# Kernel optimization log

Measured on AMD Instinct MI355X. Metric: run time of the kernel, lower is better.

Reference implementation:

```python
import jax, jax.numpy as jnp
import numpy as np

N, E = 50000, 600000
IN_DIM, HID, OUT = 512, 256, 64
NEG_SLOPE = 0.2  # pyg GATConv default negative_slope


def setup_inputs() -> dict:
    key = jax.random.key(0)
    ks = jax.random.split(key, 6)
    features = jax.random.normal(ks[0], (N, IN_DIM), jnp.float32)
    edge_index = jax.random.randint(ks[1], (2, E), 0, N)
    W1 = jax.random.normal(ks[2], (IN_DIM, HID), jnp.float32) * (1.0 / np.sqrt(IN_DIM))
    W2 = jax.random.normal(ks[3], (HID, OUT), jnp.float32) * (1.0 / np.sqrt(HID))
    att_src = jax.random.normal(ks[4], (HID,), jnp.float32) * 0.1
    att_dst = jax.random.normal(ks[5], (HID,), jnp.float32) * 0.1
    return {"features": features, "W1": W1, "W2": W2,
            "att_src": att_src, "att_dst": att_dst, "edge_index": edge_index}


def _gat_propagate(h_pre, a_src, a_dst, src, dst, n):
    """STAGATE GATConv message passing (heads=1, concat=False, no self loops).

    Per-edge logit = leaky_relu(alpha_src[src] + alpha_dst[dst]),
    softmax over edges sharing the same dst, scatter-add of weighted src feats.
    """
    logits = jax.nn.leaky_relu(a_src[src] + a_dst[dst], NEG_SLOPE)        # [E]
    m = jax.ops.segment_max(logits, dst, num_segments=n)                   # [N]
    ex = jnp.exp(logits - m[dst])                                          # [E]
    denom = jax.ops.segment_sum(ex, dst, num_segments=n)                   # [N]
    w = ex / (denom[dst] + 1e-16)                                          # [E], pyg softmax eps
    return jax.ops.segment_sum(h_pre[src] * w[:, None], dst, num_segments=n)  # [N, C]


def reference(features, W1, W2, att_src, att_dst, edge_index):
    src, dst = edge_index[0], edge_index[1]
    n = features.shape[0]
    # conv1: attention computed and cached (self.attentions)
    hp1 = features @ W1                      # [N, HID]
    a_s = hp1 @ att_src                      # [N] per-node src attention score
    a_d = hp1 @ att_dst                      # [N] per-node dst attention score
    h1 = jax.nn.elu(_gat_propagate(hp1, a_s, a_d, src, dst, n))
    # conv2: attention=False -> plain linear
    h2 = h1 @ W2                             # [N, OUT]
    # conv3: weights = conv2.lin_src.T, tied_attention = conv1.attentions
    hp3 = h2 @ W2.T                          # [N, HID]
    h3 = jax.nn.elu(_gat_propagate(hp3, a_s, a_d, src, dst, n))
    # conv4: weights = conv1.lin_src.T, attention=False
    h4 = h3 @ W1.T                           # [N, IN_DIM]
    return (h2, h4)
```

## Files before the change

### kernel.cpp

```cpp
#include <hip/hip_runtime.h>
#include <hip/hip_bf16.h>
#include <cstdint>
#include <cstddef>

#define IN_DIM 512
#define HID 256
#define OUTD 64
#define NEG_SLOPE 0.2f

typedef __attribute__((ext_vector_type(8))) __bf16 bfrag_t;
typedef __attribute__((ext_vector_type(4))) float facc_t;
typedef __attribute__((ext_vector_type(4))) unsigned int u32x4;

__device__ __forceinline__ float bf2f(unsigned short u) {
  return __uint_as_float(((unsigned int)u) << 16);
}
__device__ __forceinline__ unsigned short f2bf(float f) {
  unsigned int x = __float_as_uint(f);
  x = (x + 0x7FFFu + ((x >> 16) & 1u)) >> 16;
  return (unsigned short)x;
}

#define GLOAD_LDS16(g, l)                                              \
  __builtin_amdgcn_global_load_lds(                                    \
      (const __attribute__((address_space(1))) void*)(g),              \
      (__attribute__((address_space(3))) void*)(l), 16, 0, 0)

template <int BM, int BN>
__global__ __launch_bounds__(256) void gemm_bt(const unsigned short* __restrict__ A,
                                               const unsigned short* __restrict__ B,
                                               void* __restrict__ Craw,
                                               unsigned short* __restrict__ Cb,
                                               int M, int N, int K, int c32) {
  constexpr int FM = BM / 32, FN = BN / 32;
  constexpr int RT = BM + BN;
  __shared__ __align__(16) unsigned short lds[RT * 32];

  const int bm0 = blockIdx.x * BM;
  const int bn0 = blockIdx.y * BN;
  const int tid = threadIdx.x;
  const int lane = tid & 63;
  const int wave = tid >> 6;
  const int wrow = (wave >> 1) * (BM / 2);
  const int wcol = (wave & 1) * (BN / 2);
  const int lr = lane & 15;
  const int quad = lane >> 4;
  const int swz = (quad ^ (lr & 3)) << 3;

  facc_t acc[FM][FN];
#pragma unroll
  for (int i = 0; i < FM; ++i)
#pragma unroll
    for (int j = 0; j < FN; ++j) acc[i][j] = (facc_t){0.f, 0.f, 0.f, 0.f};

  for (int k0 = 0; k0 < K; k0 += 32) {
    __syncthreads();
#pragma unroll
    for (int t = wave; t < RT / 16; t += 4) {
      const int r0 = t * 16;
      const int row = r0 + (lane >> 2);
      const int seg = (lane & 3) ^ (row & 3);
      const unsigned short* g;
      if (r0 < BM) {
        int gm = bm0 + row;
        if (gm >= M) gm = M - 1;
        g = A + (size_t)gm * K + k0 + seg * 8;
      } else {
        g = B + (size_t)(bn0 + row - BM) * K + k0 + seg * 8;
      }
      GLOAD_LDS16(g, lds + t * 512);
    }
    __syncthreads();

    bfrag_t a[FM], b[FN];
#pragma unroll
    for (int i = 0; i < FM; ++i)
      a[i] = *(const bfrag_t*)&lds[(wrow + i * 16 + lr) * 32 + swz];
#pragma unroll
    for (int j = 0; j < FN; ++j)
      b[j] = *(const bfrag_t*)&lds[(BM + wcol + j * 16 + lr) * 32 + swz];
#pragma unroll
    for (int i = 0; i < FM; ++i)
#pragma unroll
      for (int j = 0; j < FN; ++j)
        acc[i][j] = __builtin_amdgcn_mfma_f32_16x16x32_bf16(a[i], b[j], acc[i][j], 0, 0, 0);
  }

#pragma unroll
  for (int i = 0; i < FM; ++i)
#pragma unroll
    for (int r = 0; r < 4; ++r) {
      const int grow = bm0 + wrow + i * 16 + quad * 4 + r;
      if (grow < M) {
#pragma unroll
        for (int j = 0; j < FN; ++j) {
          const int gcol = bn0 + wcol + j * 16 + lr;
          const float v = acc[i][j][r];
          if (c32) ((float*)Craw)[(size_t)grow * N + gcol] = v;
          else ((unsigned short*)Craw)[(size_t)grow * N + gcol] = f2bf(v);
          if (Cb) Cb[(size_t)grow * N + gcol] = f2bf(v);
        }
      }
    }
}

__global__ void cvt_feat(const float* __restrict__ in, unsigned short* __restrict__ out,
                         int n8) {
  const int i = blockIdx.x * 256 + threadIdx.x;
  if (i >= n8) return;
  const float4 f0 = ((const float4*)in)[i * 2];
  const float4 f1 = ((const float4*)in)[i * 2 + 1];
  u32x4 pk;
  pk.x = (unsigned int)f2bf(f0.x) | ((unsigned int)f2bf(f0.y) << 16);
  pk.y = (unsigned int)f2bf(f0.z) | ((unsigned int)f2bf(f0.w) << 16);
  pk.z = (unsigned int)f2bf(f1.x) | ((unsigned int)f2bf(f1.y) << 16);
  pk.w = (unsigned int)f2bf(f1.z) | ((unsigned int)f2bf(f1.w) << 16);
  ((u32x4*)out)[i] = pk;
}

__global__ void cvt_straight(const float* __restrict__ in, unsigned short* __restrict__ out,
                             int nelem) {
  const int i = blockIdx.x * 256 + threadIdx.x;
  if (i < nelem) out[i] = f2bf(in[i]);
}

__global__ void transpose_cvt(const float* __restrict__ in, unsigned short* __restrict__ out,
                              int R, int C) {
  const int idx = blockIdx.x * 256 + threadIdx.x;
  if (idx >= R * C) return;
  const int r = idx / C, c = idx % C;
  out[(size_t)c * R + r] = f2bf(in[idx]);
}

__global__ __launch_bounds__(256) void rowdot(const unsigned short* __restrict__ hp,
                                              const float* __restrict__ att_s,
                                              const float* __restrict__ att_d,
                                              float* __restrict__ as_, float* __restrict__ ad_,
                                              int n) {
  const int node = blockIdx.x * 4 + (threadIdx.x >> 6);
  if (node >= n) return;
  const int lane = threadIdx.x & 63;
  const unsigned short* row = hp + (size_t)node * HID + (lane << 2);
  float s = 0.f, d = 0.f;
#pragma unroll
  for (int j = 0; j < 4; ++j) {
    const float h = bf2f(row[j]);
    s += h * att_s[(lane << 2) + j];
    d += h * att_d[(lane << 2) + j];
  }
  for (int off = 32; off > 0; off >>= 1) {
    s += __shfl_down(s, off);
    d += __shfl_down(d, off);
  }
  if (lane == 0) { as_[node] = s; ad_[node] = d; }
}

__global__ void init_nodes(float* __restrict__ denom, int* __restrict__ deg, int n) {
  const int i = blockIdx.x * 256 + threadIdx.x;
  if (i < n) {
    denom[i] = 0.f;
    deg[i] = 0;
  }
}

__global__ void edge_pass1(const int* __restrict__ src, const int* __restrict__ dst,
                           const float* __restrict__ as_, const float* __restrict__ ad_,
                           float* __restrict__ eexp, float* __restrict__ denom,
                           int* __restrict__ deg, int E, int n) {
  const int e = blockIdx.x * 256 + threadIdx.x;
  if (e >= E) return;
  const int s = src[e], d = dst[e];
  if ((unsigned)s >= (unsigned)n || (unsigned)d >= (unsigned)n) return;
  float l = as_[s] + ad_[d];
  l = l > 0.f ? l : NEG_SLOPE * l;
  const float ex = expf(fminf(l, 60.f));
  eexp[e] = ex;
  atomicAdd(&denom[d], ex);
  atomicAdd(&deg[d], 1);
}

__global__ __launch_bounds__(256) void scan_reduce(const int* __restrict__ deg,
                                                   int* __restrict__ bsum, int n) {
  __shared__ int ws4[4];
  const int tid = threadIdx.x, lane = tid & 63, wid = tid >> 6;
  const int base = blockIdx.x * 2048 + tid * 8;
  int s = 0;
#pragma unroll
  for (int j = 0; j < 8; ++j) {
    const int i = base + j;
    if (i < n) s += deg[i];
  }
  for (int off = 32; off > 0; off >>= 1) s += __shfl_down(s, off);
  if (lane == 0) ws4[wid] = s;
  __syncthreads();
  if (tid == 0) bsum[blockIdx.x] = ws4[0] + ws4[1] + ws4[2] + ws4[3];
}

__global__ __launch_bounds__(256) void scan_final(const int* __restrict__ deg,
                                                  const int* __restrict__ bsum,
                                                  int* __restrict__ row_ptr,
                                                  int* __restrict__ cursor, int n) {
  __shared__ int wsum[4];
  __shared__ int blockoff;
  const int tid = threadIdx.x, lane = tid & 63, wid = tid >> 6;
  if (wid == 0) {
    int v = (lane < blockIdx.x) ? bsum[lane] : 0;
    for (int off = 32; off > 0; off >>= 1) v += __shfl_down(v, off);
    if (lane == 0) blockoff = v;
  }
  const int base = blockIdx.x * 2048 + tid * 8;
  int v[8], s = 0;
#pragma unroll
  for (int j = 0; j < 8; ++j) {
    const int i = base + j;
    v[j] = (i < n) ? deg[i] : 0;
    s += v[j];
  }
  int ws = s;
  for (int off = 1; off < 64; off <<= 1) {
    const int t = __shfl_up(ws, off);
    if (lane >= off) ws += t;
  }
  if (lane == 63) wsum[wid] = ws;
  __syncthreads();
  int woff = 0;
  for (int w_ = 0; w_ < wid; ++w_) woff += wsum[w_];
  int run = blockoff + woff + (ws - s);
#pragma unroll
  for (int j = 0; j < 8; ++j) {
    const int i = base + j;
    if (i < n) {
      cursor[i] = run;
      row_ptr[i + 1] = run + v[j];
    }
    run += v[j];
  }
  if (blockIdx.x == 0 && tid == 0) row_ptr[0] = 0;
}

__global__ void edge_scatter(const int* __restrict__ src, const int* __restrict__ dst,
                             const float* __restrict__ eexp, const float* __restrict__ denom,
                             int* __restrict__ cursor, int* __restrict__ csr_src,
                             float* __restrict__ csr_w, int E, int n) {
  const int e = blockIdx.x * 256 + threadIdx.x;
  if (e >= E) return;
  const int s = src[e], d = dst[e];
  if ((unsigned)s >= (unsigned)n || (unsigned)d >= (unsigned)n) return;
  const float w = eexp[e] / (denom[d] + 1e-16f);
  const int pos = atomicAdd(&cursor[d], 1);
  csr_src[pos] = s;
  csr_w[pos] = w;
}

__global__ __launch_bounds__(256) void gat_prop(const unsigned short* __restrict__ hpre,
                                                const int* __restrict__ row_ptr,
                                                const int* __restrict__ csr_src,
                                                const float* __restrict__ csr_w,
                                                unsigned short* __restrict__ out, int n) {
  const int node = blockIdx.x * 4 + (threadIdx.x >> 6);
  if (node >= n) return;
  const int lane = threadIdx.x & 63;
  const int beg = row_ptr[node], end = row_ptr[node + 1];
  const unsigned short* rowbase = hpre + (size_t)(lane << 2);
  float a0 = 0.f, a1 = 0.f, a2 = 0.f, a3 = 0.f;
  int e = beg;
  for (; e + 4 <= end; e += 4) {
    const int s0 = csr_src[e], s1 = csr_src[e + 1], s2 = csr_src[e + 2], s3 = csr_src[e + 3];
    const float w0 = csr_w[e], w1 = csr_w[e + 1], w2 = csr_w[e + 2], w3 = csr_w[e + 3];
    const uint2 v0 = *(const uint2*)(rowbase + (size_t)s0 * HID);
    const uint2 v1 = *(const uint2*)(rowbase + (size_t)s1 * HID);
    const uint2 v2 = *(const uint2*)(rowbase + (size_t)s2 * HID);
    const uint2 v3 = *(const uint2*)(rowbase + (size_t)s3 * HID);
    a0 += w0 * bf2f((unsigned short)(v0.x & 0xffffu)) + w1 * bf2f((unsigned short)(v1.x & 0xffffu))
        + w2 * bf2f((unsigned short)(v2.x & 0xffffu)) + w3 * bf2f((unsigned short)(v3.x & 0xffffu));
    a1 += w0 * bf2f((unsigned short)(v0.x >> 16)) + w1 * bf2f((unsigned short)(v1.x >> 16))
        + w2 * bf2f((unsigned short)(v2.x >> 16)) + w3 * bf2f((unsigned short)(v3.x >> 16));
    a2 += w0 * bf2f((unsigned short)(v0.y & 0xffffu)) + w1 * bf2f((unsigned short)(v1.y & 0xffffu))
        + w2 * bf2f((unsigned short)(v2.y & 0xffffu)) + w3 * bf2f((unsigned short)(v3.y & 0xffffu));
    a3 += w0 * bf2f((unsigned short)(v0.y >> 16)) + w1 * bf2f((unsigned short)(v1.y >> 16))
        + w2 * bf2f((unsigned short)(v2.y >> 16)) + w3 * bf2f((unsigned short)(v3.y >> 16));
  }
  for (; e < end; ++e) {
    const int s = csr_src[e];
    const float w = csr_w[e];
    const uint2 v = *(const uint2*)(rowbase + (size_t)s * HID);
    a0 += w * bf2f((unsigned short)(v.x & 0xffffu));
    a1 += w * bf2f((unsigned short)(v.x >> 16));
    a2 += w * bf2f((unsigned short)(v.y & 0xffffu));
    a3 += w * bf2f((unsigned short)(v.y >> 16));
  }
  a0 = a0 > 0.f ? a0 : (expf(a0) - 1.f);
  a1 = a1 > 0.f ? a1 : (expf(a1) - 1.f);
  a2 = a2 > 0.f ? a2 : (expf(a2) - 1.f);
  a3 = a3 > 0.f ? a3 : (expf(a3) - 1.f);
  uint2 o;
  o.x = (unsigned int)f2bf(a0) | ((unsigned int)f2bf(a1) << 16);
  o.y = (unsigned int)f2bf(a2) | ((unsigned int)f2bf(a3) << 16);
  *(uint2*)(out + (size_t)node * HID + (lane << 2)) = o;
}

extern "C" void kernel_launch(void* const* d_in, const int* in_sizes, int n_in,
                              void* d_out, int out_size, void* d_ws, size_t ws_size,
                              hipStream_t stream) {
  const float* feat = (const float*)d_in[0];
  const float* W1 = (const float*)d_in[1];
  const float* W2 = (const float*)d_in[2];
  const float* att_s = (const float*)d_in[3];
  const float* att_d = (const float*)d_in[4];
  const int* ei = (const int*)d_in[5];
  const int N = in_sizes[0] / IN_DIM;
  const int E = in_sizes[5] / 2;
  const int* src = ei;
  const int* dst = ei + E;
  float* outf = (float*)d_out;

  unsigned short* featb = (unsigned short*)(outf + (size_t)N * OUTD);
  unsigned short* hp1 = featb + (size_t)N * IN_DIM;
  unsigned short* hp3 = hp1 + (size_t)N * HID;

  char* w = (char*)d_ws;
  size_t off = 0;
  auto alloc = [&](size_t bytes) -> void* {
    void* p = w + off;
    off += (bytes + 255) & ~(size_t)255;
    return p;
  };
  unsigned short* h1h3 = (unsigned short*)alloc((size_t)N * HID * 2);
  unsigned short* h2b = (unsigned short*)alloc((size_t)N * OUTD * 2);
  float* a_src_v = (float*)alloc((size_t)N * 4);
  float* a_dst_v = (float*)alloc((size_t)N * 4);
  float* eexp = (float*)alloc((size_t)E * 4);
  float* denom = (float*)alloc((size_t)N * 4);
  int* deg = (int*)alloc((size_t)N * 4);
  int* row_ptr = (int*)alloc((size_t)(N + 1) * 4);
  int* cursor = (int*)alloc((size_t)N * 4);
  int* bsum = (int*)alloc((size_t)64 * 4);
  int* csr_src = (int*)alloc((size_t)E * 4);
  float* csr_w = (float*)alloc((size_t)E * 4);
  unsigned short* W1T = (unsigned short*)alloc((size_t)IN_DIM * HID * 2);
  unsigned short* W1b = (unsigned short*)alloc((size_t)IN_DIM * HID * 2);
  unsigned short* W2T = (unsigned short*)alloc((size_t)HID * OUTD * 2);
  unsigned short* W2b = (unsigned short*)alloc((size_t)HID * OUTD * 2);

  const int EB = (E + 255) / 256;
  const int NB = (N + 255) / 256;
  const int MB = (N + 127) / 128;
  const int SB = (N + 2047) / 2048;

  cvt_feat<<<(N * IN_DIM / 8 + 255) / 256, 256, 0, stream>>>(feat, featb, N * IN_DIM / 8);
  transpose_cvt<<<(IN_DIM * HID + 255) / 256, 256, 0, stream>>>(W1, W1T, IN_DIM, HID);
  cvt_straight<<<(IN_DIM * HID + 255) / 256, 256, 0, stream>>>(W1, W1b, IN_DIM * HID);
  transpose_cvt<<<(HID * OUTD + 255) / 256, 256, 0, stream>>>(W2, W2T, HID, OUTD);
  cvt_straight<<<(HID * OUTD + 255) / 256, 256, 0, stream>>>(W2, W2b, HID * OUTD);

  gemm_bt<128, 128><<<dim3(MB, HID / 128), 256, 0, stream>>>(featb, W1T, hp1, nullptr,
                                                             N, HID, IN_DIM, 0);
  rowdot<<<(N + 3) / 4, 256, 0, stream>>>(hp1, att_s, att_d, a_src_v, a_dst_v, N);

  init_nodes<<<NB, 256, 0, stream>>>(denom, deg, N);
  edge_pass1<<<EB, 256, 0, stream>>>(src, dst, a_src_v, a_dst_v, eexp, denom, deg, E, N);
  scan_reduce<<<SB, 256, 0, stream>>>(deg, bsum, N);
  scan_final<<<SB, 256, 0, stream>>>(deg, bsum, row_ptr, cursor, N);
  edge_scatter<<<EB, 256, 0, stream>>>(src, dst, eexp, denom, cursor, csr_src, csr_w, E, N);

  gat_prop<<<(N + 3) / 4, 256, 0, stream>>>(hp1, row_ptr, csr_src, csr_w, h1h3, N);
  gemm_bt<128, 64><<<dim3(MB, OUTD / 64), 256, 0, stream>>>(h1h3, W2T, outf, h2b,
                                                            N, OUTD, HID, 1);
  gemm_bt<128, 128><<<dim3(MB, HID / 128), 256, 0, stream>>>(h2b, W2b, hp3, nullptr,
                                                             N, HID, OUTD, 0);
  gat_prop<<<(N + 3) / 4, 256, 0, stream>>>(hp3, row_ptr, csr_src, csr_w, h1h3, N);
  gemm_bt<128, 128><<<dim3(MB, IN_DIM / 128), 256, 0, stream>>>(h1h3, W1b,
                                                                outf + (size_t)N * OUTD,
                                                                nullptr, N, IN_DIM, HID, 1);
}
```

Measured before the change: 502.5 us.

## Propagate 64-wide h2 before W2.T projection and fuse weight conversions

Conv3 aggregation is linear, so it is reordered: the 64-wide h2 is aggregated over edges first, then multiplied by W2.T with ELU fused into the GEMM epilogue. This cuts the gather width from 256 to 64 columns in the second propagation. The 256-wide propagation now uses 16-byte loads with the two wave halves handling alternate edges, combined by a shuffle reduction. The four weight conversion kernels are merged into one. Rounding changes because the aggregation now runs on bf16 h2 instead of bf16 hp3.

```diff
diff --git a/kernel.cpp b/kernel.cpp
--- a/kernel.cpp
+++ b/kernel.cpp
@@ -31,7 +31,7 @@
                                                const unsigned short* __restrict__ B,
                                                void* __restrict__ Craw,
                                                unsigned short* __restrict__ Cb,
-                                               int M, int N, int K, int c32) {
+                                               int M, int N, int K, int c32, int act) {
   constexpr int FM = BM / 32, FN = BN / 32;
   constexpr int RT = BM + BN;
   __shared__ __align__(16) unsigned short lds[RT * 32];
@@ -95,7 +95,8 @@
 #pragma unroll
         for (int j = 0; j < FN; ++j) {
           const int gcol = bn0 + wcol + j * 16 + lr;
-          const float v = acc[i][j][r];
+          float v = acc[i][j][r];
+          if (act) v = v > 0.f ? v : (expf(v) - 1.f);
           if (c32) ((float*)Craw)[(size_t)grow * N + gcol] = v;
           else ((unsigned short*)Craw)[(size_t)grow * N + gcol] = f2bf(v);
           if (Cb) Cb[(size_t)grow * N + gcol] = f2bf(v);
@@ -118,18 +119,22 @@
   ((u32x4*)out)[i] = pk;
 }
 
-__global__ void cvt_straight(const float* __restrict__ in, unsigned short* __restrict__ out,
-                             int nelem) {
-  const int i = blockIdx.x * 256 + threadIdx.x;
-  if (i < nelem) out[i] = f2bf(in[i]);
-}
-
-__global__ void transpose_cvt(const float* __restrict__ in, unsigned short* __restrict__ out,
-                              int R, int C) {
+__global__ void cvt_weights(const float* __restrict__ W1, const float* __restrict__ W2,
+                            unsigned short* __restrict__ W1T, unsigned short* __restrict__ W1b,
+                            unsigned short* __restrict__ W2T, unsigned short* __restrict__ W2b) {
   const int idx = blockIdx.x * 256 + threadIdx.x;
-  if (idx >= R * C) return;
-  const int r = idx / C, c = idx % C;
-  out[(size_t)c * R + r] = f2bf(in[idx]);
+  if (idx < IN_DIM * HID) {
+    const unsigned short b = f2bf(W1[idx]);
+    W1b[idx] = b;
+    const int r = idx >> 8, c = idx & 255;
+    W1T[(size_t)c * IN_DIM + r] = b;
+  }
+  if (idx < HID * OUTD) {
+    const unsigned short b = f2bf(W2[idx]);
+    W2b[idx] = b;
+    const int r = idx >> 6, c = idx & 63;
+    W2T[(size_t)c * HID + r] = b;
+  }
 }
 
 __global__ __launch_bounds__(256) void rowdot(const unsigned short* __restrict__ hp,
@@ -252,51 +257,116 @@
   csr_w[pos] = w;
 }
 
-__global__ __launch_bounds__(256) void gat_prop(const unsigned short* __restrict__ hpre,
-                                                const int* __restrict__ row_ptr,
-                                                const int* __restrict__ csr_src,
-                                                const float* __restrict__ csr_w,
-                                                unsigned short* __restrict__ out, int n) {
+__global__ __launch_bounds__(256) void gat_prop256(const unsigned short* __restrict__ hpre,
+                                                   const int* __restrict__ row_ptr,
+                                                   const int* __restrict__ csr_src,
+                                                   const float* __restrict__ csr_w,
+                                                   unsigned short* __restrict__ out, int n) {
   const int node = blockIdx.x * 4 + (threadIdx.x >> 6);
   if (node >= n) return;
   const int lane = threadIdx.x & 63;
+  const int half = lane >> 5;
+  const int lh = lane & 31;
   const int beg = row_ptr[node], end = row_ptr[node + 1];
-  const unsigned short* rowbase = hpre + (size_t)(lane << 2);
+  const unsigned short* base = hpre + (lh << 3);
+  float a[8] = {0.f, 0.f, 0.f, 0.f, 0.f, 0.f, 0.f, 0.f};
+  int e = beg;
+  for (; e + 8 <= end; e += 8) {
+#pragma unroll
+    for (int u = 0; u < 4; ++u) {
+      const int e2 = e + 2 * u + half;
+      const int s = csr_src[e2];
+      const float w = csr_w[e2];
+      const u32x4 v = *(const u32x4*)(base + (size_t)s * HID);
+      a[0] += w * bf2f((unsigned short)(v.x & 0xffffu));
+      a[1] += w * bf2f((unsigned short)(v.x >> 16));
+      a[2] += w * bf2f((unsigned short)(v.y & 0xffffu));
+      a[3] += w * bf2f((unsigned short)(v.y >> 16));
+      a[4] += w * bf2f((unsigned short)(v.z & 0xffffu));
+      a[5] += w * bf2f((unsigned short)(v.z >> 16));
+      a[6] += w * bf2f((unsigned short)(v.w & 0xffffu));
+      a[7] += w * bf2f((unsigned short)(v.w >> 16));
+    }
+  }
+  for (; e < end; e += 2) {
+    const int e2 = e + half;
+    if (e2 < end) {
+      const int s = csr_src[e2];
+      const float w = csr_w[e2];
+      const u32x4 v = *(const u32x4*)(base + (size_t)s * HID);
+      a[0] += w * bf2f((unsigned short)(v.x & 0xffffu));
+      a[1] += w * bf2f((unsigned short)(v.x >> 16));
+      a[2] += w * bf2f((unsigned short)(v.y & 0xffffu));
+      a[3] += w * bf2f((unsigned short)(v.y >> 16));
+      a[4] += w * bf2f((unsigned short)(v.z & 0xffffu));
+      a[5] += w * bf2f((unsigned short)(v.z >> 16));
+      a[6] += w * bf2f((unsigned short)(v.w & 0xffffu));
+      a[7] += w * bf2f((unsigned short)(v.w >> 16));
+    }
+  }
+#pragma unroll
+  for (int i = 0; i < 8; ++i) a[i] += __shfl_xor(a[i], 32);
+  if (half == 0) {
+#pragma unroll
+    for (int i = 0; i < 8; ++i) a[i] = a[i] > 0.f ? a[i] : (expf(a[i]) - 1.f);
+    u32x4 o;
+    o.x = (unsigned int)f2bf(a[0]) | ((unsigned int)f2bf(a[1]) << 16);
+    o.y = (unsigned int)f2bf(a[2]) | ((unsigned int)f2bf(a[3]) << 16);
+    o.z = (unsigned int)f2bf(a[4]) | ((unsigned int)f2bf(a[5]) << 16);
+    o.w = (unsigned int)f2bf(a[6]) | ((unsigned int)f2bf(a[7]) << 16);
+    *(u32x4*)(out + (size_t)node * HID + (lh << 3)) = o;
+  }
+}
+
+__global__ __launch_bounds__(256) void gat_prop64(const unsigned short* __restrict__ hpre,
+                                                  const int* __restrict__ row_ptr,
+                                                  const int* __restrict__ csr_src,
+                                                  const float* __restrict__ csr_w,
+                                                  unsigned short* __restrict__ out, int n) {
+  const int node = blockIdx.x * 4 + (threadIdx.x >> 6);
+  if (node >= n) return;
+  const int lane = threadIdx.x & 63;
+  const int quad = lane >> 4;
+  const int lr = lane & 15;
+  const int beg = row_ptr[node], end = row_ptr[node + 1];
+  const unsigned short* base = hpre + (lr << 2);
   float a0 = 0.f, a1 = 0.f, a2 = 0.f, a3 = 0.f;
   int e = beg;
-  for (; e + 4 <= end; e += 4) {
-    const int s0 = csr_src[e], s1 = csr_src[e + 1], s2 = csr_src[e + 2], s3 = csr_src[e + 3];
-    const float w0 = csr_w[e], w1 = csr_w[e + 1], w2 = csr_w[e + 2], w3 = csr_w[e + 3];
-    const uint2 v0 = *(const uint2*)(rowbase + (size_t)s0 * HID);
-    const uint2 v1 = *(const uint2*)(rowbase + (size_t)s1 * HID);
-    const uint2 v2 = *(const uint2*)(rowbase + (size_t)s2 * HID);
-    const uint2 v3 = *(const uint2*)(rowbase + (size_t)s3 * HID);
-    a0 += w0 * bf2f((unsigned short)(v0.x & 0xffffu)) + w1 * bf2f((unsigned short)(v1.x & 0xffffu))
-        + w2 * bf2f((unsigned short)(v2.x & 0xffffu)) + w3 * bf2f((unsigned short)(v3.x & 0xffffu));
-    a1 += w0 * bf2f((unsigned short)(v0.x >> 16)) + w1 * bf2f((unsigned short)(v1.x >> 16))
-        + w2 * bf2f((unsigned short)(v2.x >> 16)) + w3 * bf2f((unsigned short)(v3.x >> 16));
-    a2 += w0 * bf2f((unsigned short)(v0.y & 0xffffu)) + w1 * bf2f((unsigned short)(v1.y & 0xffffu))
-        + w2 * bf2f((unsigned short)(v2.y & 0xffffu)) + w3 * bf2f((unsigned short)(v3.y & 0xffffu));
-    a3 += w0 * bf2f((unsigned short)(v0.y >> 16)) + w1 * bf2f((unsigned short)(v1.y >> 16))
-        + w2 * bf2f((unsigned short)(v2.y >> 16)) + w3 * bf2f((unsigned short)(v3.y >> 16));
-  }
-  for (; e < end; ++e) {
-    const int s = csr_src[e];
-    const float w = csr_w[e];
-    const uint2 v = *(const uint2*)(rowbase + (size_t)s * HID);
-    a0 += w * bf2f((unsigned short)(v.x & 0xffffu));
-    a1 += w * bf2f((unsigned short)(v.x >> 16));
-    a2 += w * bf2f((unsigned short)(v.y & 0xffffu));
-    a3 += w * bf2f((unsigned short)(v.y >> 16));
-  }
-  a0 = a0 > 0.f ? a0 : (expf(a0) - 1.f);
-  a1 = a1 > 0.f ? a1 : (expf(a1) - 1.f);
-  a2 = a2 > 0.f ? a2 : (expf(a2) - 1.f);
-  a3 = a3 > 0.f ? a3 : (expf(a3) - 1.f);
-  uint2 o;
-  o.x = (unsigned int)f2bf(a0) | ((unsigned int)f2bf(a1) << 16);
-  o.y = (unsigned int)f2bf(a2) | ((unsigned int)f2bf(a3) << 16);
-  *(uint2*)(out + (size_t)node * HID + (lane << 2)) = o;
+  for (; e + 8 <= end; e += 8) {
+#pragma unroll
+    for (int u = 0; u < 2; ++u) {
+      const int e2 = e + 4 * u + quad;
+      const int s = csr_src[e2];
+      const float w = csr_w[e2];
+      const uint2 v = *(const uint2*)(base + (size_t)s * OUTD);
+      a0 += w * bf2f((unsigned short)(v.x & 0xffffu));
+      a1 += w * bf2f((unsigned short)(v.x >> 16));
+      a2 += w * bf2f((unsigned short)(v.y & 0xffffu));
+      a3 += w * bf2f((unsigned short)(v.y >> 16));
+    }
+  }
+  for (; e < end; e += 4) {
+    const int e2 = e + quad;
+    if (e2 < end) {
+      const int s = csr_src[e2];
+      const float w = csr_w[e2];
+      const uint2 v = *(const uint2*)(base + (size_t)s * OUTD);
+      a0 += w * bf2f((unsigned short)(v.x & 0xffffu));
+      a1 += w * bf2f((unsigned short)(v.x >> 16));
+      a2 += w * bf2f((unsigned short)(v.y & 0xffffu));
+      a3 += w * bf2f((unsigned short)(v.y >> 16));
+    }
+  }
+  a0 += __shfl_xor(a0, 16); a0 += __shfl_xor(a0, 32);
+  a1 += __shfl_xor(a1, 16); a1 += __shfl_xor(a1, 32);
+  a2 += __shfl_xor(a2, 16); a2 += __shfl_xor(a2, 32);
+  a3 += __shfl_xor(a3, 16); a3 += __shfl_xor(a3, 32);
+  if (quad == 0) {
+    uint2 o;
+    o.x = (unsigned int)f2bf(a0) | ((unsigned int)f2bf(a1) << 16);
+    o.y = (unsigned int)f2bf(a2) | ((unsigned int)f2bf(a3) << 16);
+    *(uint2*)(out + (size_t)node * OUTD + (lr << 2)) = o;
+  }
 }
 
 extern "C" void kernel_launch(void* const* d_in, const int* in_sizes, int n_in,
@@ -316,7 +386,7 @@
 
   unsigned short* featb = (unsigned short*)(outf + (size_t)N * OUTD);
   unsigned short* hp1 = featb + (size_t)N * IN_DIM;
-  unsigned short* hp3 = hp1 + (size_t)N * HID;
+  unsigned short* g2 = hp1 + (size_t)N * HID;
 
   char* w = (char*)d_ws;
   size_t off = 0;
@@ -348,13 +418,10 @@
   const int SB = (N + 2047) / 2048;
 
   cvt_feat<<<(N * IN_DIM / 8 + 255) / 256, 256, 0, stream>>>(feat, featb, N * IN_DIM / 8);
-  transpose_cvt<<<(IN_DIM * HID + 255) / 256, 256, 0, stream>>>(W1, W1T, IN_DIM, HID);
-  cvt_straight<<<(IN_DIM * HID + 255) / 256, 256, 0, stream>>>(W1, W1b, IN_DIM * HID);
-  transpose_cvt<<<(HID * OUTD + 255) / 256, 256, 0, stream>>>(W2, W2T, HID, OUTD);
-  cvt_straight<<<(HID * OUTD + 255) / 256, 256, 0, stream>>>(W2, W2b, HID * OUTD);
+  cvt_weights<<<(IN_DIM * HID + 255) / 256, 256, 0, stream>>>(W1, W2, W1T, W1b, W2T, W2b);
 
   gemm_bt<128, 128><<<dim3(MB, HID / 128), 256, 0, stream>>>(featb, W1T, hp1, nullptr,
-                                                             N, HID, IN_DIM, 0);
+                                                             N, HID, IN_DIM, 0, 0);
   rowdot<<<(N + 3) / 4, 256, 0, stream>>>(hp1, att_s, att_d, a_src_v, a_dst_v, N);
 
   init_nodes<<<NB, 256, 0, stream>>>(denom, deg, N);
@@ -363,13 +430,13 @@
   scan_final<<<SB, 256, 0, stream>>>(deg, bsum, row_ptr, cursor, N);
   edge_scatter<<<EB, 256, 0, stream>>>(src, dst, eexp, denom, cursor, csr_src, csr_w, E, N);
 
-  gat_prop<<<(N + 3) / 4, 256, 0, stream>>>(hp1, row_ptr, csr_src, csr_w, h1h3, N);
+  gat_prop256<<<(N + 3) / 4, 256, 0, stream>>>(hp1, row_ptr, csr_src, csr_w, h1h3, N);
   gemm_bt<128, 64><<<dim3(MB, OUTD / 64), 256, 0, stream>>>(h1h3, W2T, outf, h2b,
-                                                            N, OUTD, HID, 1);
-  gemm_bt<128, 128><<<dim3(MB, HID / 128), 256, 0, stream>>>(h2b, W2b, hp3, nullptr,
-                                                             N, HID, OUTD, 0);
-  gat_prop<<<(N + 3) / 4, 256, 0, stream>>>(hp3, row_ptr, csr_src, csr_w, h1h3, N);
+                                                            N, OUTD, HID, 1, 0);
+  gat_prop64<<<(N + 3) / 4, 256, 0, stream>>>(h2b, row_ptr, csr_src, csr_w, g2, N);
+  gemm_bt<128, 128><<<dim3(MB, HID / 128), 256, 0, stream>>>(g2, W2b, h1h3, nullptr,
+                                                             N, HID, OUTD, 0, 1);
   gemm_bt<128, 128><<<dim3(MB, IN_DIM / 128), 256, 0, stream>>>(h1h3, W1b,
                                                                 outf + (size_t)N * OUTD,
-                                                                nullptr, N, IN_DIM, HID, 1);
-}
+                                                                nullptr, N, IN_DIM, HID, 1, 0);
+}
```

Measured after the change: 502.8 us. About the same (+0.1%).
